# Performance work log

Measured on AMD Instinct MI355X. Metric: run time of the kernel, lower is better.

Reference implementation:

```python
import jax, jax.numpy as jnp
import numpy as np

STAGE_NUM = 3
EPS = 1e-6
BN_EPS = 1e-5


def setup_inputs() -> dict:
    key = jax.random.key(0)
    ks = jax.random.split(key, 6)
    b, c, h, w, k = 16, 512, 64, 64, 64
    x = jax.random.normal(ks[0], (b, c, h, w), dtype=jnp.float32)
    conv1_w = jax.random.normal(ks[1], (c, c), dtype=jnp.float32) * np.sqrt(2.0 / c)
    conv1_b = jax.random.normal(ks[2], (c,), dtype=jnp.float32) * 0.01
    mu = jax.random.normal(ks[3], (c, k), dtype=jnp.float32) * np.sqrt(2.0 / k)
    mu = mu / (EPS + jnp.linalg.norm(mu, axis=0, keepdims=True))
    conv2_w = jax.random.normal(ks[4], (c, c), dtype=jnp.float32) * np.sqrt(2.0 / c)
    bn_gamma = jnp.ones((c,), dtype=jnp.float32)
    bn_beta = jnp.zeros((c,), dtype=jnp.float32)
    bn_mean = jnp.zeros((c,), dtype=jnp.float32)
    bn_var = jnp.ones((c,), dtype=jnp.float32)
    return {"x": x, "conv1_w": conv1_w, "conv1_b": conv1_b, "mu": mu,
            "conv2_w": conv2_w, "bn_gamma": bn_gamma, "bn_beta": bn_beta,
            "bn_mean": bn_mean, "bn_var": bn_var}


def _l2norm(a, axis):
    return a / (EPS + jnp.linalg.norm(a, axis=axis, keepdims=True))


def reference(x, conv1_w, conv1_b, mu, conv2_w, bn_gamma, bn_beta, bn_mean, bn_var):
    b, c, h, w = x.shape
    n = h * w
    # conv1: 1x1 conv with bias == per-pixel matmul
    x = jnp.einsum('oc,bchw->bohw', conv1_w, x) + conv1_b[None, :, None, None]
    xf = x.reshape(b, c, n)             # (b, c, n)
    x_t = xf.transpose(0, 2, 1)         # (b, n, c)
    m = mu                              # (c, k), broadcast on first iter
    z = None
    for _ in range(STAGE_NUM):
        z = jax.nn.softmax(jnp.matmul(x_t, m), axis=2)        # (b, n, k)
        z_ = z / (EPS + z.sum(axis=1, keepdims=True))          # column-normalize
        m = jnp.matmul(xf, z_)                                 # (b, c, k)
        m = _l2norm(m, axis=1)
    # EM loop is under torch.no_grad in the original
    m = jax.lax.stop_gradient(m)
    z = jax.lax.stop_gradient(z)
    rec = jnp.matmul(m, z.transpose(0, 2, 1))                  # (b, c, n)
    rec = jax.nn.relu(rec).reshape(b, c, h, w)
    # conv2: 1x1 conv (no bias) + BatchNorm (inference form, running stats)
    out = jnp.einsum('oc,bchw->bohw', conv2_w, rec)
    inv = bn_gamma / jnp.sqrt(bn_var + BN_EPS)
    out = out * inv[None, :, None, None] + (bn_beta - bn_mean * inv)[None, :, None, None]
    return out
```

## Files before the change

### kernel.cpp

```cpp
#include <hip/hip_runtime.h>
#include <stdint.h>

#define BB 16
#define CC 512
#define NN 4096
#define KC 64

typedef unsigned short ushort_t;
typedef __attribute__((ext_vector_type(8))) __bf16 bf16x8;
typedef __attribute__((ext_vector_type(4))) float f32x4;

static __device__ __forceinline__ float bu2f(ushort_t u){
  union{unsigned int i; float f;} v; v.i = ((unsigned int)u)<<16; return v.f;
}
static __device__ __forceinline__ ushort_t f2bu(float f){
  unsigned int x = __float_as_uint(f);
  return (ushort_t)((x + 0x7FFFu + ((x>>16)&1u)) >> 16);
}
static __device__ __forceinline__ ushort_t lo_part(float v, ushort_t hi){
  return f2bu(v - bu2f(hi));
}

#define MFMA16(a,b,c) __builtin_amdgcn_mfma_f32_16x16x32_bf16(a,b,c,0,0,0)

template<int ROWS>
static __device__ __forceinline__ void stage_lds(const ushort_t* __restrict__ g, int ld,
                                                 ushort_t* l, int tid){
  int wid = tid >> 6, lane = tid & 63;
  #pragma unroll
  for (int it = 0; it < ROWS/32; ++it){
    int chunk = it*4 + wid;
    int row = chunk*8 + (lane >> 3);
    int seg = (lane & 7) ^ (row & 7);
    const ushort_t* gp = g + (size_t)row*ld + seg*8;
    ushort_t* lp = l + chunk*512;
    __builtin_amdgcn_global_load_lds(
        (const __attribute__((address_space(1))) void*)gp,
        (__attribute__((address_space(3))) void*)lp, 16, 0, 0);
  }
}
static __device__ __forceinline__ bf16x8 frag_ld(const ushort_t* l, int row, int ko){
  return *(const bf16x8*)(l + row*64 + (ko ^ ((row & 7) << 3)));
}

__global__ __launch_bounds__(256) void k_transpose(const float* __restrict__ x,
    ushort_t* __restrict__ xTh, ushort_t* __restrict__ xTl, int hasLo){
  __shared__ ushort_t th[64][68];
  __shared__ ushort_t tl[64][68];
  int b = blockIdx.z, c0 = blockIdx.y*64, n0 = blockIdx.x*64;
  int r16 = threadIdx.x >> 4;
  int q4  = (threadIdx.x & 15) * 4;
  #pragma unroll
  for (int p = 0; p < 4; ++p){
    int row = r16 + p*16;
    size_t off = ((size_t)b*CC + c0 + row)*NN + n0 + q4;
    float4 v = *(const float4*)(x + off);
    ushort_t h0=f2bu(v.x), h1=f2bu(v.y), h2=f2bu(v.z), h3=f2bu(v.w);
    th[q4+0][row]=h0; th[q4+1][row]=h1; th[q4+2][row]=h2; th[q4+3][row]=h3;
    if (hasLo){
      tl[q4+0][row]=lo_part(v.x,h0); tl[q4+1][row]=lo_part(v.y,h1);
      tl[q4+2][row]=lo_part(v.z,h2); tl[q4+3][row]=lo_part(v.w,h3);
    }
  }
  __syncthreads();
  #pragma unroll
  for (int p = 0; p < 4; ++p){
    int nrow = r16 + p*16;
    size_t off = ((size_t)b*NN + n0 + nrow)*CC + c0 + q4;
    ushort4 v;
    v.x = th[nrow][q4+0]; v.y = th[nrow][q4+1]; v.z = th[nrow][q4+2]; v.w = th[nrow][q4+3];
    *(ushort4*)(xTh + off) = v;
    if (hasLo){
      ushort4 u;
      u.x = tl[nrow][q4+0]; u.y = tl[nrow][q4+1]; u.z = tl[nrow][q4+2]; u.w = tl[nrow][q4+3];
      *(ushort4*)(xTl + off) = u;
    }
  }
}

__global__ __launch_bounds__(256) void k_prep(const float* __restrict__ gamma,
    const float* __restrict__ beta, const float* __restrict__ mean,
    const float* __restrict__ var, const float* __restrict__ b1,
    const float* __restrict__ W1, const float* __restrict__ W2,
    const float* __restrict__ mu,
    float* __restrict__ bnscale, float* __restrict__ bnshift,
    float* __restrict__ b1f,
    ushort_t* __restrict__ W1h, ushort_t* __restrict__ W1l,
    ushort_t* __restrict__ W1Th, ushort_t* __restrict__ W1Tl,
    ushort_t* __restrict__ W2h, ushort_t* __restrict__ W2l,
    ushort_t* __restrict__ mTh, ushort_t* __restrict__ mTl){
  int t = blockIdx.x*256 + threadIdx.x;
  if (t < CC){
    float inv = gamma[t] * rsqrtf(var[t] + 1e-5f);
    bnscale[t] = inv;
    bnshift[t] = beta[t] - mean[t]*inv;
    b1f[t] = b1[t];
  }
  if (t < CC*CC){
    int o = t >> 9, c = t & (CC-1);
    float w1 = W1[t], w2 = W2[t];
    ushort_t h1 = f2bu(w1), h2 = f2bu(w2);
    W1h[t] = h1; W1l[t] = lo_part(w1,h1);
    W1Th[(size_t)c*CC + o] = h1; W1Tl[(size_t)c*CC + o] = lo_part(w1,h1);
    W2h[t] = h2; W2l[t] = lo_part(w2,h2);
  }
  if (t < BB*KC*CC){
    int c = t & (CC-1);
    int k = (t >> 9) & (KC-1);
    float v = mu[(size_t)c*KC + k];
    ushort_t h = f2bu(v);
    mTh[t] = h; mTl[t] = lo_part(v,h);
  }
}

__global__ __launch_bounds__(256) void k_conv1r(const ushort_t* __restrict__ W1h,
    const ushort_t* __restrict__ W1l, const float* __restrict__ bias,
    const ushort_t* __restrict__ xTh, const ushort_t* __restrict__ xTl, int hasBl,
    ushort_t* __restrict__ xfh, ushort_t* __restrict__ xfl, int hasxfl){
  __shared__ __align__(16) ushort_t sm[4*128*64];
  ushort_t* lAh = sm;
  ushort_t* lAl = sm + 128*64;
  ushort_t* lBh = sm + 2*128*64;
  ushort_t* lBl = sm + 3*128*64;
  int b = blockIdx.z, m0 = blockIdx.y*128, n0 = blockIdx.x*128;
  int tid = threadIdx.x, wid = tid>>6, lane = tid&63, quad = lane>>4, l16 = lane&15;
  int wm = wid>>1, wn = wid&1;
  f32x4 zero4 = {0.f,0.f,0.f,0.f};
  f32x4 acc[4][4];
  #pragma unroll
  for (int i=0;i<4;++i){
    #pragma unroll
    for (int j=0;j<4;++j) acc[i][j] = zero4;
  }
  const ushort_t* Aph = W1h + (size_t)m0*CC;
  const ushort_t* Apl = W1l + (size_t)m0*CC;
  const ushort_t* Bph = xTh + ((size_t)b*NN + n0)*CC;
  const ushort_t* Bpl = hasBl ? xTl + ((size_t)b*NN + n0)*CC : nullptr;
  for (int k0 = 0; k0 < CC; k0 += 64){
    stage_lds<128>(Aph + k0, CC, lAh, tid);
    stage_lds<128>(Apl + k0, CC, lAl, tid);
    stage_lds<128>(Bph + k0, CC, lBh, tid);
    if (hasBl) stage_lds<128>(Bpl + k0, CC, lBl, tid);
    __syncthreads();
    #pragma unroll
    for (int kk = 0; kk < 64; kk += 32){
      bf16x8 ah[4], al[4], bh[4], bl[4];
      #pragma unroll
      for (int f=0; f<4; ++f){
        ah[f] = frag_ld(lAh, wm*64 + f*16 + l16, kk + quad*8);
        al[f] = frag_ld(lAl, wm*64 + f*16 + l16, kk + quad*8);
        bh[f] = frag_ld(lBh, wn*64 + f*16 + l16, kk + quad*8);
      }
      if (hasBl){
        #pragma unroll
        for (int f=0; f<4; ++f) bl[f] = frag_ld(lBl, wn*64 + f*16 + l16, kk + quad*8);
      }
      #pragma unroll
      for (int i=0;i<4;++i){
        #pragma unroll
        for (int j=0;j<4;++j){
          acc[i][j] = MFMA16(ah[i], bh[j], acc[i][j]);
          acc[i][j] = MFMA16(al[i], bh[j], acc[i][j]);
        }
      }
      if (hasBl){
        #pragma unroll
        for (int i=0;i<4;++i){
          #pragma unroll
          for (int j=0;j<4;++j) acc[i][j] = MFMA16(ah[i], bl[j], acc[i][j]);
        }
      }
    }
    __syncthreads();
  }
  ushort_t* ct = sm;
  float vals[4][4][4];
  #pragma unroll
  for (int i=0;i<4;++i){
    #pragma unroll
    for (int r=0;r<4;++r){
      int m = wm*64 + i*16 + quad*4 + r;
      float bv = bias[m0 + m];
      #pragma unroll
      for (int j=0;j<4;++j){
        float v = acc[i][j][r] + bv;
        vals[i][j][r] = v;
        ct[m*132 + (wn*64 + j*16 + l16)] = f2bu(v);
      }
    }
  }
  __syncthreads();
  {
    ushort_t* xfp = xfh + (size_t)b*CC*NN + (size_t)m0*NN + n0;
    #pragma unroll
    for (int i = 0; i < 16; ++i){
      int idx = tid + i*256;
      int m = idx >> 5, j4 = (idx & 31)*4;
      *(ushort4*)(xfp + (size_t)m*NN + j4) = *(ushort4*)(ct + m*132 + j4);
    }
  }
  if (hasxfl){
    __syncthreads();
    #pragma unroll
    for (int i=0;i<4;++i){
      #pragma unroll
      for (int r=0;r<4;++r){
        int m = wm*64 + i*16 + quad*4 + r;
        #pragma unroll
        for (int j=0;j<4;++j){
          float v = vals[i][j][r];
          ct[m*132 + (wn*64 + j*16 + l16)] = lo_part(v, f2bu(v));
        }
      }
    }
    __syncthreads();
    ushort_t* xfp = xfl + (size_t)b*CC*NN + (size_t)m0*NN + n0;
    #pragma unroll
    for (int i = 0; i < 16; ++i){
      int idx = tid + i*256;
      int m = idx >> 5, j4 = (idx & 31)*4;
      *(ushort4*)(xfp + (size_t)m*NN + j4) = *(ushort4*)(ct + m*132 + j4);
    }
  }
}

__global__ __launch_bounds__(256) void k_q(const float* __restrict__ b1f,
    const ushort_t* __restrict__ mTh, const ushort_t* __restrict__ mTl,
    float* __restrict__ qout){
  int b = blockIdx.x, t = threadIdx.x;
  int k = t & 63, seg = t >> 6;
  const ushort_t* mh = mTh + (size_t)b*KC*CC + (size_t)k*CC;
  const ushort_t* ml = mTl + (size_t)b*KC*CC + (size_t)k*CC;
  float s = 0.f;
  #pragma unroll 4
  for (int o = seg*128; o < seg*128 + 128; ++o)
    s += b1f[o]*(bu2f(mh[o]) + bu2f(ml[o]));
  __shared__ float red[256];
  red[t] = s; __syncthreads();
  if (seg == 0) qout[b*KC + k] = red[k] + red[64+k] + red[128+k] + red[192+k];
}

__global__ __launch_bounds__(256) void k_wm2(const ushort_t* __restrict__ W1Th,
    const ushort_t* __restrict__ W1Tl,
    const ushort_t* __restrict__ mTh, const ushort_t* __restrict__ mTl,
    ushort_t* __restrict__ PTh, ushort_t* __restrict__ PTl){
  __shared__ __align__(16) ushort_t sm[4*64*64];
  ushort_t* lAh = sm;
  ushort_t* lAl = sm + 4096;
  ushort_t* lBh = sm + 8192;
  ushort_t* lBl = sm + 12288;
  int c0 = blockIdx.x*64, bk0 = blockIdx.y*64;
  int tid = threadIdx.x, wid = tid>>6, lane = tid&63, quad = lane>>4, l16 = lane&15;
  f32x4 zero4 = {0.f,0.f,0.f,0.f};
  f32x4 acc[4];
  #pragma unroll
  for (int j=0;j<4;++j) acc[j] = zero4;
  const ushort_t* Aph = W1Th + (size_t)c0*CC;
  const ushort_t* Apl = W1Tl + (size_t)c0*CC;
  const ushort_t* Bph = mTh + (size_t)bk0*CC;
  const ushort_t* Bpl = mTl + (size_t)bk0*CC;
  for (int k0 = 0; k0 < CC; k0 += 64){
    stage_lds<64>(Aph + k0, CC, lAh, tid);
    stage_lds<64>(Apl + k0, CC, lAl, tid);
    stage_lds<64>(Bph + k0, CC, lBh, tid);
    stage_lds<64>(Bpl + k0, CC, lBl, tid);
    __syncthreads();
    #pragma unroll
    for (int kk = 0; kk < 64; kk += 32){
      bf16x8 ah, al, bh[4], bl[4];
      ah = frag_ld(lAh, wid*16 + l16, kk + quad*8);
      al = frag_ld(lAl, wid*16 + l16, kk + quad*8);
      #pragma unroll
      for (int f=0; f<4; ++f){
        bh[f] = frag_ld(lBh, f*16 + l16, kk + quad*8);
        bl[f] = frag_ld(lBl, f*16 + l16, kk + quad*8);
      }
      #pragma unroll
      for (int j=0;j<4;++j){
        acc[j] = MFMA16(ah, bh[j], acc[j]);
        acc[j] = MFMA16(ah, bl[j], acc[j]);
        acc[j] = MFMA16(al, bh[j], acc[j]);
      }
    }
    __syncthreads();
  }
  int cbase = c0 + wid*16 + quad*4;
  #pragma unroll
  for (int j=0;j<4;++j){
    int bk = bk0 + j*16 + l16;
    ushort4 vh, vl;
    float a0=acc[j][0], a1=acc[j][1], a2=acc[j][2], a3=acc[j][3];
    vh.x=f2bu(a0); vh.y=f2bu(a1); vh.z=f2bu(a2); vh.w=f2bu(a3);
    vl.x=lo_part(a0,vh.x); vl.y=lo_part(a1,vh.y); vl.z=lo_part(a2,vh.z); vl.w=lo_part(a3,vh.w);
    size_t off = (size_t)bk*CC + cbase;
    *(ushort4*)(PTh + off) = vh;
    *(ushort4*)(PTl + off) = vl;
  }
}

__global__ __launch_bounds__(256) void k_logits(const ushort_t* __restrict__ xTh,
    const ushort_t* __restrict__ xTl, int hasAl,
    const ushort_t* __restrict__ PTh, const ushort_t* __restrict__ PTl,
    const float* __restrict__ q,
    ushort_t* __restrict__ zh, ushort_t* __restrict__ zl, int writeZ,
    ushort_t* __restrict__ zTh, ushort_t* __restrict__ zTl,
    float* __restrict__ colsum){
  __shared__ __align__(16) ushort_t sm[2*128*64 + 2*64*64];
  ushort_t* lAh = sm;
  ushort_t* lAl = sm + 128*64;
  ushort_t* lBh = sm + 2*128*64;
  ushort_t* lBl = sm + 2*128*64 + 64*64;
  int b = blockIdx.y, n0 = blockIdx.x*128;
  int tid = threadIdx.x, wid = tid>>6, lane = tid&63, quad = lane>>4, l16 = lane&15;
  f32x4 zero4 = {0.f,0.f,0.f,0.f};
  f32x4 acc[2][4];
  #pragma unroll
  for (int i=0;i<2;++i){
    #pragma unroll
    for (int j=0;j<4;++j) acc[i][j] = zero4;
  }
  const ushort_t* Aph = xTh + ((size_t)b*NN + n0)*CC;
  const ushort_t* Apl = hasAl ? xTl + ((size_t)b*NN + n0)*CC : nullptr;
  const ushort_t* Bph = PTh + (size_t)b*KC*CC;
  const ushort_t* Bpl = PTl + (size_t)b*KC*CC;
  for (int k0 = 0; k0 < CC; k0 += 64){
    stage_lds<128>(Aph + k0, CC, lAh, tid);
    if (hasAl) stage_lds<128>(Apl + k0, CC, lAl, tid);
    stage_lds<64>(Bph + k0, CC, lBh, tid);
    stage_lds<64>(Bpl + k0, CC, lBl, tid);
    __syncthreads();
    #pragma unroll
    for (int kk = 0; kk < 64; kk += 32){
      bf16x8 ah[2], al[2], bh[4], bl[4];
      #pragma unroll
      for (int f=0; f<2; ++f){
        ah[f] = frag_ld(lAh, wid*32 + f*16 + l16, kk + quad*8);
        if (hasAl) al[f] = frag_ld(lAl, wid*32 + f*16 + l16, kk + quad*8);
      }
      #pragma unroll
      for (int f=0; f<4; ++f){
        bh[f] = frag_ld(lBh, f*16 + l16, kk + quad*8);
        bl[f] = frag_ld(lBl, f*16 + l16, kk + quad*8);
      }
      #pragma unroll
      for (int i=0;i<2;++i){
        #pragma unroll
        for (int j=0;j<4;++j){
          acc[i][j] = MFMA16(ah[i], bh[j], acc[i][j]);
          acc[i][j] = MFMA16(ah[i], bl[j], acc[i][j]);
        }
      }
      if (hasAl){
        #pragma unroll
        for (int i=0;i<2;++i){
          #pragma unroll
          for (int j=0;j<4;++j) acc[i][j] = MFMA16(al[i], bh[j], acc[i][j]);
        }
      }
    }
    __syncthreads();
  }
  float qv[4];
  #pragma unroll
  for (int j=0;j<4;++j) qv[j] = q[b*KC + j*16 + l16];
  #pragma unroll
  for (int i=0;i<2;++i){
    #pragma unroll
    for (int r=0;r<4;++r){
      #pragma unroll
      for (int j=0;j<4;++j) acc[i][j][r] += qv[j];
      float mx = fmaxf(fmaxf(acc[i][0][r], acc[i][1][r]), fmaxf(acc[i][2][r], acc[i][3][r]));
      mx = fmaxf(mx, __shfl_xor(mx, 1));
      mx = fmaxf(mx, __shfl_xor(mx, 2));
      mx = fmaxf(mx, __shfl_xor(mx, 4));
      mx = fmaxf(mx, __shfl_xor(mx, 8));
      float e0 = __expf(acc[i][0][r]-mx), e1 = __expf(acc[i][1][r]-mx);
      float e2 = __expf(acc[i][2][r]-mx), e3 = __expf(acc[i][3][r]-mx);
      float s = e0+e1+e2+e3;
      s += __shfl_xor(s, 1); s += __shfl_xor(s, 2);
      s += __shfl_xor(s, 4); s += __shfl_xor(s, 8);
      float inv = 1.0f/s;
      acc[i][0][r] = e0*inv; acc[i][1][r] = e1*inv;
      acc[i][2][r] = e2*inv; acc[i][3][r] = e3*inv;
    }
  }
  #pragma unroll
  for (int j=0;j<4;++j){
    float p = 0.f;
    #pragma unroll
    for (int i=0;i<2;++i){
      #pragma unroll
      for (int r=0;r<4;++r) p += acc[i][j][r];
    }
    p += __shfl_xor(p, 16); p += __shfl_xor(p, 32);
    if (lane < 16) atomicAdd(&colsum[b*KC + j*16 + l16], p);
  }
  #pragma unroll
  for (int i=0;i<2;++i){
    int nbase = wid*32 + i*16 + quad*4;
    #pragma unroll
    for (int j=0;j<4;++j){
      int k = j*16 + l16;
      ushort4 vh, vl;
      float a0=acc[i][j][0], a1=acc[i][j][1], a2=acc[i][j][2], a3=acc[i][j][3];
      vh.x=f2bu(a0); vh.y=f2bu(a1); vh.z=f2bu(a2); vh.w=f2bu(a3);
      vl.x=lo_part(a0,vh.x); vl.y=lo_part(a1,vh.y); vl.z=lo_part(a2,vh.z); vl.w=lo_part(a3,vh.w);
      size_t zoff = ((size_t)b*KC + k)*NN + n0 + nbase;
      *(ushort4*)(zTh + zoff) = vh;
      *(ushort4*)(zTl + zoff) = vl;
      if (writeZ){
        const ushort_t* ph = (const ushort_t*)&vh;
        const ushort_t* pl = (const ushort_t*)&vl;
        #pragma unroll
        for (int r=0;r<4;++r){
          size_t o = ((size_t)b*NN + n0 + nbase + r)*KC + k;
          zh[o] = ph[r]; zl[o] = pl[r];
        }
      }
    }
  }
}

__global__ __launch_bounds__(256) void k_mgemm(const ushort_t* __restrict__ xfh,
    const ushort_t* __restrict__ xfl, int hasAl,
    const ushort_t* __restrict__ zTh, const ushort_t* __restrict__ zTl,
    float* __restrict__ m_part){
  __shared__ __align__(16) ushort_t sm[2*128*64 + 2*64*64];
  ushort_t* lAh = sm;
  ushort_t* lAl = sm + 128*64;
  ushort_t* lBh = sm + 2*128*64;
  ushort_t* lBl = sm + 2*128*64 + 64*64;
  int c0 = blockIdx.x*128, slice = blockIdx.y, b = blockIdx.z;
  int tid = threadIdx.x, wid = tid>>6, lane = tid&63, quad = lane>>4, l16 = lane&15;
  f32x4 zero4 = {0.f,0.f,0.f,0.f};
  f32x4 acc[2][4];
  #pragma unroll
  for (int i=0;i<2;++i){
    #pragma unroll
    for (int j=0;j<4;++j) acc[i][j] = zero4;
  }
  const ushort_t* Aph = xfh + ((size_t)b*CC + c0)*NN + slice*512;
  const ushort_t* Apl = hasAl ? xfl + ((size_t)b*CC + c0)*NN + slice*512 : nullptr;
  const ushort_t* Bph = zTh + (size_t)b*KC*NN + slice*512;
  const ushort_t* Bpl = zTl + (size_t)b*KC*NN + slice*512;
  for (int k0 = 0; k0 < 512; k0 += 64){
    stage_lds<128>(Aph + k0, NN, lAh, tid);
    if (hasAl) stage_lds<128>(Apl + k0, NN, lAl, tid);
    stage_lds<64>(Bph + k0, NN, lBh, tid);
    stage_lds<64>(Bpl + k0, NN, lBl, tid);
    __syncthreads();
    #pragma unroll
    for (int kk = 0; kk < 64; kk += 32){
      bf16x8 ah[2], al[2], bh[4], bl[4];
      #pragma unroll
      for (int f=0; f<2; ++f){
        ah[f] = frag_ld(lAh, wid*32 + f*16 + l16, kk + quad*8);
        if (hasAl) al[f] = frag_ld(lAl, wid*32 + f*16 + l16, kk + quad*8);
      }
      #pragma unroll
      for (int f=0; f<4; ++f){
        bh[f] = frag_ld(lBh, f*16 + l16, kk + quad*8);
        bl[f] = frag_ld(lBl, f*16 + l16, kk + quad*8);
      }
      #pragma unroll
      for (int i=0;i<2;++i){
        #pragma unroll
        for (int j=0;j<4;++j){
          acc[i][j] = MFMA16(ah[i], bh[j], acc[i][j]);
          acc[i][j] = MFMA16(ah[i], bl[j], acc[i][j]);
        }
      }
      if (hasAl){
        #pragma unroll
        for (int i=0;i<2;++i){
          #pragma unroll
          for (int j=0;j<4;++j) acc[i][j] = MFMA16(al[i], bh[j], acc[i][j]);
        }
      }
    }
    __syncthreads();
  }
  #pragma unroll
  for (int i=0;i<2;++i){
    int c = c0 + wid*32 + i*16 + quad*4;
    #pragma unroll
    for (int j=0;j<4;++j){
      int k = j*16 + l16;
      *(f32x4*)(m_part + (((size_t)slice*BB + b)*KC + k)*CC + c) = acc[i][j];
    }
  }
}

__global__ __launch_bounds__(256) void k_mnorm(const float* __restrict__ m_part,
    const float* __restrict__ colsum, const float* __restrict__ b1f,
    ushort_t* __restrict__ mch, ushort_t* __restrict__ mcl,
    ushort_t* __restrict__ mTh, ushort_t* __restrict__ mTl,
    float* __restrict__ qout){
  int k = blockIdx.x, b = blockIdx.y, t = threadIdx.x;
  float v0 = 0.f, v1 = 0.f;
  #pragma unroll
  for (int s = 0; s < 8; ++s){
    const float* p = m_part + (((size_t)s*BB + b)*KC + k)*CC;
    v0 += p[t]; v1 += p[t+256];
  }
  float sk = 1.0f/(1e-6f + colsum[b*KC + k]);
  v0 *= sk; v1 *= sk;
  float ss = v0*v0 + v1*v1;
  #pragma unroll
  for (int off = 1; off < 64; off <<= 1) ss += __shfl_xor(ss, off);
  __shared__ float red[4];
  if ((t&63) == 0) red[t>>6] = ss;
  __syncthreads();
  float inv = 1.0f/(1e-6f + sqrtf(red[0]+red[1]+red[2]+red[3]));
  v0 *= inv; v1 *= inv;
  ushort_t h0 = f2bu(v0), h1 = f2bu(v1);
  ushort_t l0 = lo_part(v0,h0), l1 = lo_part(v1,h1);
  size_t to = ((size_t)b*KC + k)*CC + t;
  mTh[to] = h0; mTh[to+256] = h1;
  mTl[to] = l0; mTl[to+256] = l1;
  size_t co = ((size_t)b*CC + t)*KC + k;
  mch[co] = h0; mch[co + (size_t)256*KC] = h1;
  mcl[co] = l0; mcl[co + (size_t)256*KC] = l1;
  float qs = b1f[t]*(bu2f(h0)+bu2f(l0)) + b1f[t+256]*(bu2f(h1)+bu2f(l1));
  #pragma unroll
  for (int off = 1; off < 64; off <<= 1) qs += __shfl_xor(qs, off);
  __shared__ float red2[4];
  __syncthreads();
  if ((t&63) == 0) red2[t>>6] = qs;
  __syncthreads();
  if (t == 0) qout[b*KC + k] = red2[0]+red2[1]+red2[2]+red2[3];
}

__global__ __launch_bounds__(256) void k_rec(const ushort_t* __restrict__ zh,
    const ushort_t* __restrict__ zl,
    const ushort_t* __restrict__ mch, const ushort_t* __restrict__ mcl,
    ushort_t* __restrict__ recTh, ushort_t* __restrict__ recTl){
  __shared__ __align__(16) ushort_t sm[4*128*64];
  ushort_t* lAh = sm;
  ushort_t* lAl = sm + 128*64;
  ushort_t* lBh = sm + 2*128*64;
  ushort_t* lBl = sm + 3*128*64;
  int n0 = blockIdx.x*128, c0 = blockIdx.y*128, b = blockIdx.z;
  int tid = threadIdx.x, wid = tid>>6, lane = tid&63, quad = lane>>4, l16 = lane&15;
  int wm = wid>>1, wn = wid&1;
  f32x4 zero4 = {0.f,0.f,0.f,0.f};
  f32x4 acc[4][4];
  #pragma unroll
  for (int i=0;i<4;++i){
    #pragma unroll
    for (int j=0;j<4;++j) acc[i][j] = zero4;
  }
  stage_lds<128>(zh + ((size_t)b*NN + n0)*KC, KC, lAh, tid);
  stage_lds<128>(zl + ((size_t)b*NN + n0)*KC, KC, lAl, tid);
  stage_lds<128>(mch + ((size_t)b*CC + c0)*KC, KC, lBh, tid);
  stage_lds<128>(mcl + ((size_t)b*CC + c0)*KC, KC, lBl, tid);
  __syncthreads();
  #pragma unroll
  for (int kk = 0; kk < 64; kk += 32){
    bf16x8 ah[4], al[4], bh[4], bl[4];
    #pragma unroll
    for (int f=0; f<4; ++f){
      ah[f] = frag_ld(lAh, wm*64 + f*16 + l16, kk + quad*8);
      al[f] = frag_ld(lAl, wm*64 + f*16 + l16, kk + quad*8);
      bh[f] = frag_ld(lBh, wn*64 + f*16 + l16, kk + quad*8);
      bl[f] = frag_ld(lBl, wn*64 + f*16 + l16, kk + quad*8);
    }
    #pragma unroll
    for (int i=0;i<4;++i){
      #pragma unroll
      for (int j=0;j<4;++j){
        acc[i][j] = MFMA16(ah[i], bh[j], acc[i][j]);
        acc[i][j] = MFMA16(ah[i], bl[j], acc[i][j]);
        acc[i][j] = MFMA16(al[i], bh[j], acc[i][j]);
      }
    }
  }
  __syncthreads();
  ushort_t* ct = sm;
  #pragma unroll
  for (int i=0;i<4;++i){
    #pragma unroll
    for (int r=0;r<4;++r){
      int m = wm*64 + i*16 + quad*4 + r;
      #pragma unroll
      for (int j=0;j<4;++j)
        ct[m*132 + (wn*64 + j*16 + l16)] = f2bu(fmaxf(acc[i][j][r], 0.f));
    }
  }
  __syncthreads();
  {
    ushort_t* rp = recTh + ((size_t)b*NN + n0)*CC + c0;
    #pragma unroll
    for (int i = 0; i < 16; ++i){
      int idx = tid + i*256;
      int m = idx >> 5, j4 = (idx & 31)*4;
      *(ushort4*)(rp + (size_t)m*CC + j4) = *(ushort4*)(ct + m*132 + j4);
    }
  }
  __syncthreads();
  #pragma unroll
  for (int i=0;i<4;++i){
    #pragma unroll
    for (int r=0;r<4;++r){
      int m = wm*64 + i*16 + quad*4 + r;
      #pragma unroll
      for (int j=0;j<4;++j){
        float v = fmaxf(acc[i][j][r], 0.f);
        ct[m*132 + (wn*64 + j*16 + l16)] = lo_part(v, f2bu(v));
      }
    }
  }
  __syncthreads();
  {
    ushort_t* rp = recTl + ((size_t)b*NN + n0)*CC + c0;
    #pragma unroll
    for (int i = 0; i < 16; ++i){
      int idx = tid + i*256;
      int m = idx >> 5, j4 = (idx & 31)*4;
      *(ushort4*)(rp + (size_t)m*CC + j4) = *(ushort4*)(ct + m*132 + j4);
    }
  }
}

__global__ __launch_bounds__(256) void k_conv2(const ushort_t* __restrict__ W2h,
    const ushort_t* __restrict__ W2l,
    const ushort_t* __restrict__ recTh, const ushort_t* __restrict__ recTl,
    const float* __restrict__ bnscale, const float* __restrict__ bnshift,
    float* __restrict__ out){
  __shared__ __align__(16) ushort_t sm[4*128*64];
  ushort_t* lAh = sm;
  ushort_t* lAl = sm + 128*64;
  ushort_t* lBh = sm + 2*128*64;
  ushort_t* lBl = sm + 3*128*64;
  int b = blockIdx.z, m0 = blockIdx.y*128, n0 = blockIdx.x*128;
  int tid = threadIdx.x, wid = tid>>6, lane = tid&63, quad = lane>>4, l16 = lane&15;
  int wm = wid>>1, wn = wid&1;
  f32x4 zero4 = {0.f,0.f,0.f,0.f};
  f32x4 acc[4][4];
  #pragma unroll
  for (int i=0;i<4;++i){
    #pragma unroll
    for (int j=0;j<4;++j) acc[i][j] = zero4;
  }
  const ushort_t* Aph = W2h + (size_t)m0*CC;
  const ushort_t* Apl = W2l + (size_t)m0*CC;
  const ushort_t* Bph = recTh + ((size_t)b*NN + n0)*CC;
  const ushort_t* Bpl = recTl + ((size_t)b*NN + n0)*CC;
  for (int k0 = 0; k0 < CC; k0 += 64){
    stage_lds<128>(Aph + k0, CC, lAh, tid);
    stage_lds<128>(Apl + k0, CC, lAl, tid);
    stage_lds<128>(Bph + k0, CC, lBh, tid);
    stage_lds<128>(Bpl + k0, CC, lBl, tid);
    __syncthreads();
    #pragma unroll
    for (int kk = 0; kk < 64; kk += 32){
      bf16x8 ah[4], al[4], bh[4], bl[4];
      #pragma unroll
      for (int f=0; f<4; ++f){
        ah[f] = frag_ld(lAh, wm*64 + f*16 + l16, kk + quad*8);
        al[f] = frag_ld(lAl, wm*64 + f*16 + l16, kk + quad*8);
        bh[f] = frag_ld(lBh, wn*64 + f*16 + l16, kk + quad*8);
        bl[f] = frag_ld(lBl, wn*64 + f*16 + l16, kk + quad*8);
      }
      #pragma unroll
      for (int i=0;i<4;++i){
        #pragma unroll
        for (int j=0;j<4;++j){
          acc[i][j] = MFMA16(ah[i], bh[j], acc[i][j]);
          acc[i][j] = MFMA16(ah[i], bl[j], acc[i][j]);
          acc[i][j] = MFMA16(al[i], bh[j], acc[i][j]);
        }
      }
    }
    __syncthreads();
  }
  size_t base = (size_t)b*CC*NN;
  #pragma unroll
  for (int i=0;i<4;++i){
    #pragma unroll
    for (int r=0;r<4;++r){
      int m = m0 + wm*64 + i*16 + quad*4 + r;
      float sc = bnscale[m], sh = bnshift[m];
      #pragma unroll
      for (int j=0;j<4;++j){
        int nn = n0 + wn*64 + j*16 + l16;
        out[base + (size_t)m*NN + nn] = acc[i][j][r]*sc + sh;
      }
    }
  }
}

extern "C" void kernel_launch(void* const* d_in, const int* in_sizes, int n_in,
                              void* d_out, int out_size, void* d_ws, size_t ws_size,
                              hipStream_t stream) {
  (void)in_sizes; (void)n_in; (void)out_size;
  const float* x     = (const float*)d_in[0];
  const float* W1    = (const float*)d_in[1];
  const float* b1    = (const float*)d_in[2];
  const float* mu    = (const float*)d_in[3];
  const float* W2    = (const float*)d_in[4];
  const float* gamma = (const float*)d_in[5];
  const float* beta  = (const float*)d_in[6];
  const float* mean  = (const float*)d_in[7];
  const float* var   = (const float*)d_in[8];
  float* out = (float*)d_out;

  const size_t big = (size_t)BB*NN*CC*2;
  const size_t zsz = (size_t)BB*NN*KC*2;
  const size_t msz = (size_t)BB*KC*CC*2;
  char* w = (char*)d_ws;
  ushort_t* xTh  = (ushort_t*)w;  w += big;
  ushort_t* xfh  = (ushort_t*)w;  w += big;
  ushort_t* zh   = (ushort_t*)w;  w += zsz;
  ushort_t* zl   = (ushort_t*)w;  w += zsz;
  ushort_t* zTh  = (ushort_t*)w;  w += zsz;
  ushort_t* zTl  = (ushort_t*)w;  w += zsz;
  float*    m_part = (float*)w;   w += (size_t)8*BB*KC*CC*4;
  ushort_t* mTh  = (ushort_t*)w;  w += msz;
  ushort_t* mTl  = (ushort_t*)w;  w += msz;
  ushort_t* mch  = (ushort_t*)w;  w += msz;
  ushort_t* mcl  = (ushort_t*)w;  w += msz;
  ushort_t* PTh  = (ushort_t*)w;  w += msz;
  ushort_t* PTl  = (ushort_t*)w;  w += msz;
  ushort_t* W1h  = (ushort_t*)w;  w += (size_t)CC*CC*2;
  ushort_t* W1l  = (ushort_t*)w;  w += (size_t)CC*CC*2;
  ushort_t* W1Th = (ushort_t*)w;  w += (size_t)CC*CC*2;
  ushort_t* W1Tl = (ushort_t*)w;  w += (size_t)CC*CC*2;
  ushort_t* W2h  = (ushort_t*)w;  w += (size_t)CC*CC*2;
  ushort_t* W2l  = (ushort_t*)w;  w += (size_t)CC*CC*2;
  float*    bnscale = (float*)w;  w += 2048;
  float*    bnshift = (float*)w;  w += 2048;
  float*    b1f  = (float*)w;     w += 2048;
  float*    colsum = (float*)w;   w += (size_t)BB*KC*4;
  float*    qbuf = (float*)w;     w += (size_t)BB*KC*4;
  ushort_t* xTl = nullptr; ushort_t* xfl = nullptr;
  size_t used = (size_t)(w - (char*)d_ws);
  if (used + big <= ws_size){ xTl = (ushort_t*)w; w += big; used += big; }
  if (used + big <= ws_size){ xfl = (ushort_t*)w; w += big; used += big; }
  int hasxTl = xTl != nullptr, hasxfl = xfl != nullptr;
  ushort_t* recTh = xfh;
  ushort_t* recTl = xTh;

  k_transpose<<<dim3(NN/64, CC/64, BB), 256, 0, stream>>>(x, xTh, xTl, hasxTl);
  k_prep<<<dim3((BB*KC*CC + 255)/256), 256, 0, stream>>>(gamma, beta, mean, var, b1,
      W1, W2, mu, bnscale, bnshift, b1f, W1h, W1l, W1Th, W1Tl, W2h, W2l, mTh, mTl);
  k_conv1r<<<dim3(NN/128, CC/128, BB), 256, 0, stream>>>(W1h, W1l, b1f, xTh, xTl, hasxTl,
      xfh, xfl, hasxfl);
  k_q<<<dim3(BB), 256, 0, stream>>>(b1f, mTh, mTl, qbuf);
  for (int it = 0; it < 3; ++it){
    (void)hipMemsetAsync(colsum, 0, (size_t)BB*KC*4, stream);
    k_wm2<<<dim3(CC/64, BB*KC/64), 256, 0, stream>>>(W1Th, W1Tl, mTh, mTl, PTh, PTl);
    k_logits<<<dim3(NN/128, BB), 256, 0, stream>>>(xTh, xTl, hasxTl, PTh, PTl, qbuf,
        zh, zl, (it == 2) ? 1 : 0, zTh, zTl, colsum);
    k_mgemm<<<dim3(CC/128, 8, BB), 256, 0, stream>>>(xfh, xfl, hasxfl, zTh, zTl, m_part);
    k_mnorm<<<dim3(KC, BB), 256, 0, stream>>>(m_part, colsum, b1f, mch, mcl, mTh, mTl, qbuf);
  }
  k_rec<<<dim3(NN/128, CC/128, BB), 256, 0, stream>>>(zh, zl, mch, mcl, recTh, recTl);
  k_conv2<<<dim3(NN/128, CC/128, BB), 256, 0, stream>>>(W2h, W2l, recTh, recTl,
      bnscale, bnshift, out);
}
```

Measured before the change: 806.2 us.

## Drop conv1 GEMM by applying W1 to the small EM statistics instead

Removes the full conv1 GEMM over all pixels. The M-step now multiplies raw x (in channel-major bf16 hi/lo form, written by the transpose kernel) by z, then applies W1 plus a bias term scaled by the column sum to the small (b,k,c) result in a new k_wm3 GEMM. A merge kernel and a fused L2-norm/q kernel replace k_mnorm, and colsum zeroing moves into kernels instead of a memset. This trades one large GEMM for a few extra small kernel launches per iteration, and reorders the arithmetic, which may change rounding.

```diff
diff --git a/kernel.cpp b/kernel.cpp
--- a/kernel.cpp
+++ b/kernel.cpp
@@ -44,12 +44,14 @@
 }
 
 __global__ __launch_bounds__(256) void k_transpose(const float* __restrict__ x,
-    ushort_t* __restrict__ xTh, ushort_t* __restrict__ xTl, int hasLo){
+    ushort_t* __restrict__ xTh, ushort_t* __restrict__ xTl, int hasLo,
+    ushort_t* __restrict__ xch, ushort_t* __restrict__ xcl, int hasClo){
   __shared__ ushort_t th[64][68];
   __shared__ ushort_t tl[64][68];
   int b = blockIdx.z, c0 = blockIdx.y*64, n0 = blockIdx.x*64;
   int r16 = threadIdx.x >> 4;
   int q4  = (threadIdx.x & 15) * 4;
+  int needLo = hasLo | hasClo;
   #pragma unroll
   for (int p = 0; p < 4; ++p){
     int row = r16 + p*16;
@@ -57,9 +59,17 @@
     float4 v = *(const float4*)(x + off);
     ushort_t h0=f2bu(v.x), h1=f2bu(v.y), h2=f2bu(v.z), h3=f2bu(v.w);
     th[q4+0][row]=h0; th[q4+1][row]=h1; th[q4+2][row]=h2; th[q4+3][row]=h3;
-    if (hasLo){
-      tl[q4+0][row]=lo_part(v.x,h0); tl[q4+1][row]=lo_part(v.y,h1);
-      tl[q4+2][row]=lo_part(v.z,h2); tl[q4+3][row]=lo_part(v.w,h3);
+    ushort_t l0=0,l1=0,l2=0,l3=0;
+    if (needLo){
+      l0=lo_part(v.x,h0); l1=lo_part(v.y,h1);
+      l2=lo_part(v.z,h2); l3=lo_part(v.w,h3);
+      tl[q4+0][row]=l0; tl[q4+1][row]=l1; tl[q4+2][row]=l2; tl[q4+3][row]=l3;
+    }
+    ushort4 vh; vh.x=h0; vh.y=h1; vh.z=h2; vh.w=h3;
+    *(ushort4*)(xch + off) = vh;
+    if (hasClo){
+      ushort4 ul; ul.x=l0; ul.y=l1; ul.z=l2; ul.w=l3;
+      *(ushort4*)(xcl + off) = ul;
     }
   }
   __syncthreads();
@@ -113,121 +123,11 @@
   }
 }
 
-__global__ __launch_bounds__(256) void k_conv1r(const ushort_t* __restrict__ W1h,
-    const ushort_t* __restrict__ W1l, const float* __restrict__ bias,
-    const ushort_t* __restrict__ xTh, const ushort_t* __restrict__ xTl, int hasBl,
-    ushort_t* __restrict__ xfh, ushort_t* __restrict__ xfl, int hasxfl){
-  __shared__ __align__(16) ushort_t sm[4*128*64];
-  ushort_t* lAh = sm;
-  ushort_t* lAl = sm + 128*64;
-  ushort_t* lBh = sm + 2*128*64;
-  ushort_t* lBl = sm + 3*128*64;
-  int b = blockIdx.z, m0 = blockIdx.y*128, n0 = blockIdx.x*128;
-  int tid = threadIdx.x, wid = tid>>6, lane = tid&63, quad = lane>>4, l16 = lane&15;
-  int wm = wid>>1, wn = wid&1;
-  f32x4 zero4 = {0.f,0.f,0.f,0.f};
-  f32x4 acc[4][4];
-  #pragma unroll
-  for (int i=0;i<4;++i){
-    #pragma unroll
-    for (int j=0;j<4;++j) acc[i][j] = zero4;
-  }
-  const ushort_t* Aph = W1h + (size_t)m0*CC;
-  const ushort_t* Apl = W1l + (size_t)m0*CC;
-  const ushort_t* Bph = xTh + ((size_t)b*NN + n0)*CC;
-  const ushort_t* Bpl = hasBl ? xTl + ((size_t)b*NN + n0)*CC : nullptr;
-  for (int k0 = 0; k0 < CC; k0 += 64){
-    stage_lds<128>(Aph + k0, CC, lAh, tid);
-    stage_lds<128>(Apl + k0, CC, lAl, tid);
-    stage_lds<128>(Bph + k0, CC, lBh, tid);
-    if (hasBl) stage_lds<128>(Bpl + k0, CC, lBl, tid);
-    __syncthreads();
-    #pragma unroll
-    for (int kk = 0; kk < 64; kk += 32){
-      bf16x8 ah[4], al[4], bh[4], bl[4];
-      #pragma unroll
-      for (int f=0; f<4; ++f){
-        ah[f] = frag_ld(lAh, wm*64 + f*16 + l16, kk + quad*8);
-        al[f] = frag_ld(lAl, wm*64 + f*16 + l16, kk + quad*8);
-        bh[f] = frag_ld(lBh, wn*64 + f*16 + l16, kk + quad*8);
-      }
-      if (hasBl){
-        #pragma unroll
-        for (int f=0; f<4; ++f) bl[f] = frag_ld(lBl, wn*64 + f*16 + l16, kk + quad*8);
-      }
-      #pragma unroll
-      for (int i=0;i<4;++i){
-        #pragma unroll
-        for (int j=0;j<4;++j){
-          acc[i][j] = MFMA16(ah[i], bh[j], acc[i][j]);
-          acc[i][j] = MFMA16(al[i], bh[j], acc[i][j]);
-        }
-      }
-      if (hasBl){
-        #pragma unroll
-        for (int i=0;i<4;++i){
-          #pragma unroll
-          for (int j=0;j<4;++j) acc[i][j] = MFMA16(ah[i], bl[j], acc[i][j]);
-        }
-      }
-    }
-    __syncthreads();
-  }
-  ushort_t* ct = sm;
-  float vals[4][4][4];
-  #pragma unroll
-  for (int i=0;i<4;++i){
-    #pragma unroll
-    for (int r=0;r<4;++r){
-      int m = wm*64 + i*16 + quad*4 + r;
-      float bv = bias[m0 + m];
-      #pragma unroll
-      for (int j=0;j<4;++j){
-        float v = acc[i][j][r] + bv;
-        vals[i][j][r] = v;
-        ct[m*132 + (wn*64 + j*16 + l16)] = f2bu(v);
-      }
-    }
-  }
-  __syncthreads();
-  {
-    ushort_t* xfp = xfh + (size_t)b*CC*NN + (size_t)m0*NN + n0;
-    #pragma unroll
-    for (int i = 0; i < 16; ++i){
-      int idx = tid + i*256;
-      int m = idx >> 5, j4 = (idx & 31)*4;
-      *(ushort4*)(xfp + (size_t)m*NN + j4) = *(ushort4*)(ct + m*132 + j4);
-    }
-  }
-  if (hasxfl){
-    __syncthreads();
-    #pragma unroll
-    for (int i=0;i<4;++i){
-      #pragma unroll
-      for (int r=0;r<4;++r){
-        int m = wm*64 + i*16 + quad*4 + r;
-        #pragma unroll
-        for (int j=0;j<4;++j){
-          float v = vals[i][j][r];
-          ct[m*132 + (wn*64 + j*16 + l16)] = lo_part(v, f2bu(v));
-        }
-      }
-    }
-    __syncthreads();
-    ushort_t* xfp = xfl + (size_t)b*CC*NN + (size_t)m0*NN + n0;
-    #pragma unroll
-    for (int i = 0; i < 16; ++i){
-      int idx = tid + i*256;
-      int m = idx >> 5, j4 = (idx & 31)*4;
-      *(ushort4*)(xfp + (size_t)m*NN + j4) = *(ushort4*)(ct + m*132 + j4);
-    }
-  }
-}
-
 __global__ __launch_bounds__(256) void k_q(const float* __restrict__ b1f,
     const ushort_t* __restrict__ mTh, const ushort_t* __restrict__ mTl,
-    float* __restrict__ qout){
+    float* __restrict__ qout, float* __restrict__ colsum){
   int b = blockIdx.x, t = threadIdx.x;
+  if (t < KC) colsum[b*KC + t] = 0.f;
   int k = t & 63, seg = t >> 6;
   const ushort_t* mh = mTh + (size_t)b*KC*CC + (size_t)k*CC;
   const ushort_t* ml = mTl + (size_t)b*KC*CC + (size_t)k*CC;
@@ -421,10 +321,10 @@
   }
 }
 
-__global__ __launch_bounds__(256) void k_mgemm(const ushort_t* __restrict__ xfh,
-    const ushort_t* __restrict__ xfl, int hasAl,
+__global__ __launch_bounds__(256) void k_mgemm(const ushort_t* __restrict__ xch,
+    const ushort_t* __restrict__ xcl, int hasAl,
     const ushort_t* __restrict__ zTh, const ushort_t* __restrict__ zTl,
-    float* __restrict__ m_part){
+    float* __restrict__ y_part){
   __shared__ __align__(16) ushort_t sm[2*128*64 + 2*64*64];
   ushort_t* lAh = sm;
   ushort_t* lAl = sm + 128*64;
@@ -439,8 +339,8 @@
     #pragma unroll
     for (int j=0;j<4;++j) acc[i][j] = zero4;
   }
-  const ushort_t* Aph = xfh + ((size_t)b*CC + c0)*NN + slice*512;
-  const ushort_t* Apl = hasAl ? xfl + ((size_t)b*CC + c0)*NN + slice*512 : nullptr;
+  const ushort_t* Aph = xch + ((size_t)b*CC + c0)*NN + slice*512;
+  const ushort_t* Apl = hasAl ? xcl + ((size_t)b*CC + c0)*NN + slice*512 : nullptr;
   const ushort_t* Bph = zTh + (size_t)b*KC*NN + slice*512;
   const ushort_t* Bpl = zTl + (size_t)b*KC*NN + slice*512;
   for (int k0 = 0; k0 < 512; k0 += 64){
@@ -486,25 +386,92 @@
     #pragma unroll
     for (int j=0;j<4;++j){
       int k = j*16 + l16;
-      *(f32x4*)(m_part + (((size_t)slice*BB + b)*KC + k)*CC + c) = acc[i][j];
-    }
-  }
-}
-
-__global__ __launch_bounds__(256) void k_mnorm(const float* __restrict__ m_part,
-    const float* __restrict__ colsum, const float* __restrict__ b1f,
+      *(f32x4*)(y_part + (((size_t)slice*BB + b)*KC + k)*CC + c) = acc[i][j];
+    }
+  }
+}
+
+__global__ __launch_bounds__(256) void k_ymerge(const float* __restrict__ y_part,
+    const float* __restrict__ colsum,
+    ushort_t* __restrict__ yh, ushort_t* __restrict__ yl){
+  int k = blockIdx.x, b = blockIdx.y, t = threadIdx.x;
+  float v0 = 0.f, v1 = 0.f;
+  #pragma unroll
+  for (int s = 0; s < 8; ++s){
+    const float* p = y_part + (((size_t)s*BB + b)*KC + k)*CC;
+    v0 += p[t]; v1 += p[t+256];
+  }
+  float sk = 1.0f/(1e-6f + colsum[b*KC + k]);
+  v0 *= sk; v1 *= sk;
+  ushort_t h0 = f2bu(v0), h1 = f2bu(v1);
+  size_t o = (size_t)(b*KC + k)*CC + t;
+  yh[o] = h0; yh[o+256] = h1;
+  yl[o] = lo_part(v0,h0); yl[o+256] = lo_part(v1,h1);
+}
+
+__global__ __launch_bounds__(256) void k_wm3(const ushort_t* __restrict__ W1h,
+    const ushort_t* __restrict__ W1l,
+    const ushort_t* __restrict__ yh, const ushort_t* __restrict__ yl,
+    float* __restrict__ m_pre){
+  __shared__ __align__(16) ushort_t sm[4*64*64];
+  ushort_t* lAh = sm;
+  ushort_t* lAl = sm + 4096;
+  ushort_t* lBh = sm + 8192;
+  ushort_t* lBl = sm + 12288;
+  int o0 = blockIdx.x*64, bk0 = blockIdx.y*64;
+  int tid = threadIdx.x, wid = tid>>6, lane = tid&63, quad = lane>>4, l16 = lane&15;
+  f32x4 zero4 = {0.f,0.f,0.f,0.f};
+  f32x4 acc[4];
+  #pragma unroll
+  for (int j=0;j<4;++j) acc[j] = zero4;
+  const ushort_t* Aph = W1h + (size_t)o0*CC;
+  const ushort_t* Apl = W1l + (size_t)o0*CC;
+  const ushort_t* Bph = yh + (size_t)bk0*CC;
+  const ushort_t* Bpl = yl + (size_t)bk0*CC;
+  for (int k0 = 0; k0 < CC; k0 += 64){
+    stage_lds<64>(Aph + k0, CC, lAh, tid);
+    stage_lds<64>(Apl + k0, CC, lAl, tid);
+    stage_lds<64>(Bph + k0, CC, lBh, tid);
+    stage_lds<64>(Bpl + k0, CC, lBl, tid);
+    __syncthreads();
+    #pragma unroll
+    for (int kk = 0; kk < 64; kk += 32){
+      bf16x8 ah, al, bh[4], bl[4];
+      ah = frag_ld(lAh, wid*16 + l16, kk + quad*8);
+      al = frag_ld(lAl, wid*16 + l16, kk + quad*8);
+      #pragma unroll
+      for (int f=0; f<4; ++f){
+        bh[f] = frag_ld(lBh, f*16 + l16, kk + quad*8);
+        bl[f] = frag_ld(lBl, f*16 + l16, kk + quad*8);
+      }
+      #pragma unroll
+      for (int j=0;j<4;++j){
+        acc[j] = MFMA16(ah, bh[j], acc[j]);
+        acc[j] = MFMA16(ah, bl[j], acc[j]);
+        acc[j] = MFMA16(al, bh[j], acc[j]);
+      }
+    }
+    __syncthreads();
+  }
+  int obase = o0 + wid*16 + quad*4;
+  #pragma unroll
+  for (int j=0;j<4;++j){
+    int bk = bk0 + j*16 + l16;
+    *(f32x4*)(m_pre + (size_t)bk*CC + obase) = acc[j];
+  }
+}
+
+__global__ __launch_bounds__(256) void k_l2q(const float* __restrict__ m_pre,
+    float* __restrict__ colsum, const float* __restrict__ b1f,
     ushort_t* __restrict__ mch, ushort_t* __restrict__ mcl,
     ushort_t* __restrict__ mTh, ushort_t* __restrict__ mTl,
     float* __restrict__ qout){
   int k = blockIdx.x, b = blockIdx.y, t = threadIdx.x;
-  float v0 = 0.f, v1 = 0.f;
-  #pragma unroll
-  for (int s = 0; s < 8; ++s){
-    const float* p = m_part + (((size_t)s*BB + b)*KC + k)*CC;
-    v0 += p[t]; v1 += p[t+256];
-  }
-  float sk = 1.0f/(1e-6f + colsum[b*KC + k]);
-  v0 *= sk; v1 *= sk;
+  int bk = b*KC + k;
+  float cs = colsum[bk];
+  float bfac = cs/(1e-6f + cs);
+  float v0 = m_pre[(size_t)bk*CC + t]       + b1f[t]*bfac;
+  float v1 = m_pre[(size_t)bk*CC + t + 256] + b1f[t+256]*bfac;
   float ss = v0*v0 + v1*v1;
   #pragma unroll
   for (int off = 1; off < 64; off <<= 1) ss += __shfl_xor(ss, off);
@@ -515,7 +482,7 @@
   v0 *= inv; v1 *= inv;
   ushort_t h0 = f2bu(v0), h1 = f2bu(v1);
   ushort_t l0 = lo_part(v0,h0), l1 = lo_part(v1,h1);
-  size_t to = ((size_t)b*KC + k)*CC + t;
+  size_t to = (size_t)bk*CC + t;
   mTh[to] = h0; mTh[to+256] = h1;
   mTl[to] = l0; mTl[to+256] = l1;
   size_t co = ((size_t)b*CC + t)*KC + k;
@@ -528,7 +495,10 @@
   __syncthreads();
   if ((t&63) == 0) red2[t>>6] = qs;
   __syncthreads();
-  if (t == 0) qout[b*KC + k] = red2[0]+red2[1]+red2[2]+red2[3];
+  if (t == 0){
+    qout[bk] = red2[0]+red2[1]+red2[2]+red2[3];
+    colsum[bk] = 0.f;
+  }
 }
 
 __global__ __launch_bounds__(256) void k_rec(const ushort_t* __restrict__ zh,
@@ -710,18 +680,21 @@
   const size_t msz = (size_t)BB*KC*CC*2;
   char* w = (char*)d_ws;
   ushort_t* xTh  = (ushort_t*)w;  w += big;
-  ushort_t* xfh  = (ushort_t*)w;  w += big;
+  ushort_t* xch  = (ushort_t*)w;  w += big;
   ushort_t* zh   = (ushort_t*)w;  w += zsz;
   ushort_t* zl   = (ushort_t*)w;  w += zsz;
   ushort_t* zTh  = (ushort_t*)w;  w += zsz;
   ushort_t* zTl  = (ushort_t*)w;  w += zsz;
-  float*    m_part = (float*)w;   w += (size_t)8*BB*KC*CC*4;
+  float*    y_part = (float*)w;   w += (size_t)8*BB*KC*CC*4;
+  float*    m_pre  = (float*)w;   w += (size_t)BB*KC*CC*4;
   ushort_t* mTh  = (ushort_t*)w;  w += msz;
   ushort_t* mTl  = (ushort_t*)w;  w += msz;
   ushort_t* mch  = (ushort_t*)w;  w += msz;
   ushort_t* mcl  = (ushort_t*)w;  w += msz;
   ushort_t* PTh  = (ushort_t*)w;  w += msz;
   ushort_t* PTl  = (ushort_t*)w;  w += msz;
+  ushort_t* yh   = (ushort_t*)w;  w += msz;
+  ushort_t* yl   = (ushort_t*)w;  w += msz;
   ushort_t* W1h  = (ushort_t*)w;  w += (size_t)CC*CC*2;
   ushort_t* W1l  = (ushort_t*)w;  w += (size_t)CC*CC*2;
   ushort_t* W1Th = (ushort_t*)w;  w += (size_t)CC*CC*2;
@@ -733,27 +706,27 @@
   float*    b1f  = (float*)w;     w += 2048;
   float*    colsum = (float*)w;   w += (size_t)BB*KC*4;
   float*    qbuf = (float*)w;     w += (size_t)BB*KC*4;
-  ushort_t* xTl = nullptr; ushort_t* xfl = nullptr;
+  ushort_t* xTl = nullptr; ushort_t* xcl = nullptr;
   size_t used = (size_t)(w - (char*)d_ws);
   if (used + big <= ws_size){ xTl = (ushort_t*)w; w += big; used += big; }
-  if (used + big <= ws_size){ xfl = (ushort_t*)w; w += big; used += big; }
-  int hasxTl = xTl != nullptr, hasxfl = xfl != nullptr;
-  ushort_t* recTh = xfh;
+  if (used + big <= ws_size){ xcl = (ushort_t*)w; w += big; used += big; }
+  int hasxTl = xTl != nullptr, hasxcl = xcl != nullptr;
+  ushort_t* recTh = xch;
   ushort_t* recTl = xTh;
 
-  k_transpose<<<dim3(NN/64, CC/64, BB), 256, 0, stream>>>(x, xTh, xTl, hasxTl);
+  k_transpose<<<dim3(NN/64, CC/64, BB), 256, 0, stream>>>(x, xTh, xTl, hasxTl,
+      xch, xcl, hasxcl);
   k_prep<<<dim3((BB*KC*CC + 255)/256), 256, 0, stream>>>(gamma, beta, mean, var, b1,
       W1, W2, mu, bnscale, bnshift, b1f, W1h, W1l, W1Th, W1Tl, W2h, W2l, mTh, mTl);
-  k_conv1r<<<dim3(NN/128, CC/128, BB), 256, 0, stream>>>(W1h, W1l, b1f, xTh, xTl, hasxTl,
-      xfh, xfl, hasxfl);
-  k_q<<<dim3(BB), 256, 0, stream>>>(b1f, mTh, mTl, qbuf);
+  k_q<<<dim3(BB), 256, 0, stream>>>(b1f, mTh, mTl, qbuf, colsum);
   for (int it = 0; it < 3; ++it){
-    (void)hipMemsetAsync(colsum, 0, (size_t)BB*KC*4, stream);
     k_wm2<<<dim3(CC/64, BB*KC/64), 256, 0, stream>>>(W1Th, W1Tl, mTh, mTl, PTh, PTl);
     k_logits<<<dim3(NN/128, BB), 256, 0, stream>>>(xTh, xTl, hasxTl, PTh, PTl, qbuf,
         zh, zl, (it == 2) ? 1 : 0, zTh, zTl, colsum);
-    k_mgemm<<<dim3(CC/128, 8, BB), 256, 0, stream>>>(xfh, xfl, hasxfl, zTh, zTl, m_part);
-    k_mnorm<<<dim3(KC, BB), 256, 0, stream>>>(m_part, colsum, b1f, mch, mcl, mTh, mTl, qbuf);
+    k_mgemm<<<dim3(CC/128, 8, BB), 256, 0, stream>>>(xch, xcl, hasxcl, zTh, zTl, y_part);
+    k_ymerge<<<dim3(KC, BB), 256, 0, stream>>>(y_part, colsum, yh, yl);
+    k_wm3<<<dim3(CC/64, BB*KC/64), 256, 0, stream>>>(W1h, W1l, yh, yl, m_pre);
+    k_l2q<<<dim3(KC, BB), 256, 0, stream>>>(m_pre, colsum, b1f, mch, mcl, mTh, mTl, qbuf);
   }
   k_rec<<<dim3(NN/128, CC/128, BB), 256, 0, stream>>>(zh, zl, mch, mcl, recTh, recTl);
   k_conv2<<<dim3(NN/128, CC/128, BB), 256, 0, stream>>>(W2h, W2l, recTh, recTl,
```

New measurement: 752.9 us. 1.07x faster.
